# Optimization experiments

Hardware: AMD Instinct MI355X
Metric: run time of the kernel (lower is better)

The kernel has to match this reference:

```python
import jax, jax.numpy as jnp
import numpy as np

N = 4_000_000
EPS = 1e-6

# Quaternion layout: (w, x, y, z)

def _qmul(q1, q2):
    w1, v1 = q1[..., :1], q1[..., 1:]
    w2, v2 = q2[..., :1], q2[..., 1:]
    w = w1 * w2 - jnp.sum(v1 * v2, axis=-1, keepdims=True)
    v = w1 * v2 + w2 * v1 + jnp.cross(v1, v2)
    return jnp.concatenate([w, v], axis=-1)

def _qinv(q):
    # unit quaternion inverse = conjugate
    return q * jnp.array([1.0, -1.0, -1.0, -1.0], dtype=q.dtype)

def _qlog(q):
    # SO(3) log map: returns tangent vector theta * axis, shape [..., 3]
    w, v = q[..., 0], q[..., 1:]
    nv = jnp.linalg.norm(v, axis=-1)
    small = nv < EPS
    nv_safe = jnp.where(small, 1.0, nv)
    theta = 2.0 * jnp.arctan2(nv, w)
    # small-angle limit: theta/nv -> 2/w
    scale = jnp.where(small, 2.0 / w, theta / nv_safe)
    return v * scale[..., None]

def setup_inputs() -> dict:
    key = jax.random.key(0)
    k1, k2 = jax.random.split(key)
    a = jax.random.normal(k1, (N, 4), dtype=jnp.float32)
    a = a / jnp.linalg.norm(a, axis=-1, keepdims=True)
    idd = jax.random.normal(k2, (N, 4), dtype=jnp.float32)
    idd = idd / jnp.linalg.norm(idd, axis=-1, keepdims=True)
    return {"a": a, "idd": idd}

def reference(a, idd):
    # (a.Inv() @ idd).Log().norm()
    rel = _qmul(_qinv(a), idd)          # [N,4] relative rotation
    tangent = _qlog(rel)                 # [N,3] log map
    return jnp.linalg.norm(tangent)      # scalar Frobenius norm
```

## Files before the change

### kernel.cpp

```cpp
#include <hip/hip_runtime.h>
#include <math.h>

#define BLOCK 256
#define UNROLL 12
#define WTILE (64 * UNROLL)

typedef float vfloat4 __attribute__((ext_vector_type(4)));

__device__ __forceinline__ float theta_sq(vfloat4 qa, vfloat4 qb) {
    float w1 = qa.x, x1 = -qa.y, y1 = -qa.z, z1 = -qa.w;
    float w2 = qb.x, x2 = qb.y,  y2 = qb.z,  z2 = qb.w;
    float w  = w1*w2 - (x1*x2 + y1*y2 + z1*z2);
    float vx = w1*x2 + w2*x1 + (y1*z2 - z1*y2);
    float vy = w1*y2 + w2*y1 + (z1*x2 - x1*z2);
    float vz = w1*z2 + w2*z1 + (x1*y2 - y1*x2);
    float nv2 = vx*vx + vy*vy + vz*vz;
    float nv  = sqrtf(nv2);
    if (nv < 1e-6f) {
        float s = 2.0f / w;
        return nv2 * s * s;
    }
    float rn = rsqrtf(w*w + nv2);
    float c  = w * rn;
    float ac = fabsf(c);
    float p  = ((-0.0187293f*ac + 0.0742610f)*ac - 0.2121144f)*ac + 1.5707288f;
    float r  = sqrtf(fmaxf(1.0f - ac, 0.0f)) * p;
    float acosc = (c >= 0.0f) ? r : (3.14159265358979f - r);
    float theta = 2.0f * acosc;
    return theta * theta;
}

__global__ __launch_bounds__(BLOCK) void geo_loss_kernel(
        const vfloat4* __restrict__ a,
        const vfloat4* __restrict__ idd,
        float* __restrict__ ws, int n) {
    const int tid  = threadIdx.x;
    const int lane = tid & 63;
    const int gw   = (blockIdx.x * BLOCK + tid) >> 6;
    const int wbase = gw * WTILE;
    float acc = 0.0f;

    if (wbase + WTILE <= n) {
        vfloat4 qa[UNROLL], qb[UNROLL];
        #pragma unroll
        for (int k = 0; k < UNROLL; k++)
            qa[k] = __builtin_nontemporal_load(&a[wbase + k * 64 + lane]);
        #pragma unroll
        for (int k = 0; k < UNROLL; k++)
            qb[k] = __builtin_nontemporal_load(&idd[wbase + k * 64 + lane]);
        #pragma unroll
        for (int k = 0; k < UNROLL; k++)
            acc += theta_sq(qa[k], qb[k]);
    } else if (wbase < n) {
        for (int k = 0; k < UNROLL; k++) {
            int idx = wbase + k * 64 + lane;
            if (idx < n) acc += theta_sq(a[idx], idd[idx]);
        }
    }

    #pragma unroll
    for (int off = 32; off > 0; off >>= 1)
        acc += __shfl_down(acc, off, 64);
    __shared__ float smem[BLOCK / 64];
    int wid = tid >> 6;
    if (lane == 0) smem[wid] = acc;
    __syncthreads();
    if (tid == 0) {
        float s = smem[0] + smem[1] + smem[2] + smem[3];
        atomicAdd(ws, s);
    }
}

__global__ void finalize_kernel(const float* __restrict__ ws,
                                float* __restrict__ out) {
    out[0] = sqrtf(ws[0]);
}

extern "C" void kernel_launch(void* const* d_in, const int* in_sizes, int n_in,
                              void* d_out, int out_size, void* d_ws, size_t ws_size,
                              hipStream_t stream) {
    const vfloat4* a   = (const vfloat4*)d_in[0];
    const vfloat4* idd = (const vfloat4*)d_in[1];
    int n = in_sizes[0] / 4;
    float* ws = (float*)d_ws;

    (void)hipMemsetAsync(ws, 0, sizeof(float), stream);

    int nwaves = (n + WTILE - 1) / WTILE;
    int grid   = (nwaves + (BLOCK / 64) - 1) / (BLOCK / 64);
    geo_loss_kernel<<<grid, BLOCK, 0, stream>>>(a, idd, ws, n);
    finalize_kernel<<<1, 1, 0, stream>>>(ws, (float*)d_out);
}
```

Baseline: 145.5 us.

## Replace atomic accumulation with per-block partials and drop memset and nontemporal loads

Each block now writes its partial sum to its own workspace slot instead of doing an atomicAdd on a single float. A 256-thread finalize kernel then reduces all partials and takes the square root. This removes the hipMemsetAsync launch and the contention on one atomic address. Loads also switch from nontemporal vector loads to plain float4 loads, which changes the cache policy on the streamed inputs.

```diff
diff --git a/kernel.cpp b/kernel.cpp
--- a/kernel.cpp
+++ b/kernel.cpp
@@ -5,9 +5,7 @@
 #define UNROLL 12
 #define WTILE (64 * UNROLL)
 
-typedef float vfloat4 __attribute__((ext_vector_type(4)));
-
-__device__ __forceinline__ float theta_sq(vfloat4 qa, vfloat4 qb) {
+__device__ __forceinline__ float theta_sq(float4 qa, float4 qb) {
     float w1 = qa.x, x1 = -qa.y, y1 = -qa.z, z1 = -qa.w;
     float w2 = qb.x, x2 = qb.y,  y2 = qb.z,  z2 = qb.w;
     float w  = w1*w2 - (x1*x2 + y1*y2 + z1*z2);
@@ -31,9 +29,9 @@
 }
 
 __global__ __launch_bounds__(BLOCK) void geo_loss_kernel(
-        const vfloat4* __restrict__ a,
-        const vfloat4* __restrict__ idd,
-        float* __restrict__ ws, int n) {
+        const float4* __restrict__ a,
+        const float4* __restrict__ idd,
+        float* __restrict__ partials, int n) {
     const int tid  = threadIdx.x;
     const int lane = tid & 63;
     const int gw   = (blockIdx.x * BLOCK + tid) >> 6;
@@ -41,16 +39,13 @@
     float acc = 0.0f;
 
     if (wbase + WTILE <= n) {
-        vfloat4 qa[UNROLL], qb[UNROLL];
+        float4 qa[UNROLL], qb[UNROLL];
         #pragma unroll
-        for (int k = 0; k < UNROLL; k++)
-            qa[k] = __builtin_nontemporal_load(&a[wbase + k * 64 + lane]);
+        for (int k = 0; k < UNROLL; k++) qa[k] = a[wbase + k * 64 + lane];
         #pragma unroll
-        for (int k = 0; k < UNROLL; k++)
-            qb[k] = __builtin_nontemporal_load(&idd[wbase + k * 64 + lane]);
+        for (int k = 0; k < UNROLL; k++) qb[k] = idd[wbase + k * 64 + lane];
         #pragma unroll
-        for (int k = 0; k < UNROLL; k++)
-            acc += theta_sq(qa[k], qb[k]);
+        for (int k = 0; k < UNROLL; k++) acc += theta_sq(qa[k], qb[k]);
     } else if (wbase < n) {
         for (int k = 0; k < UNROLL; k++) {
             int idx = wbase + k * 64 + lane;
@@ -65,29 +60,38 @@
     int wid = tid >> 6;
     if (lane == 0) smem[wid] = acc;
     __syncthreads();
-    if (tid == 0) {
-        float s = smem[0] + smem[1] + smem[2] + smem[3];
-        atomicAdd(ws, s);
-    }
+    if (tid == 0)
+        partials[blockIdx.x] = smem[0] + smem[1] + smem[2] + smem[3];
 }
 
-__global__ void finalize_kernel(const float* __restrict__ ws,
-                                float* __restrict__ out) {
-    out[0] = sqrtf(ws[0]);
+__global__ __launch_bounds__(BLOCK) void finalize_kernel(
+        const float* __restrict__ partials,
+        float* __restrict__ out, int nparts) {
+    float acc = 0.0f;
+    for (int i = threadIdx.x; i < nparts; i += BLOCK)
+        acc += partials[i];
+    #pragma unroll
+    for (int off = 32; off > 0; off >>= 1)
+        acc += __shfl_down(acc, off, 64);
+    __shared__ float smem[BLOCK / 64];
+    int lane = threadIdx.x & 63;
+    int wid  = threadIdx.x >> 6;
+    if (lane == 0) smem[wid] = acc;
+    __syncthreads();
+    if (threadIdx.x == 0)
+        out[0] = sqrtf(smem[0] + smem[1] + smem[2] + smem[3]);
 }
 
 extern "C" void kernel_launch(void* const* d_in, const int* in_sizes, int n_in,
                               void* d_out, int out_size, void* d_ws, size_t ws_size,
                               hipStream_t stream) {
-    const vfloat4* a   = (const vfloat4*)d_in[0];
-    const vfloat4* idd = (const vfloat4*)d_in[1];
+    const float4* a   = (const float4*)d_in[0];
+    const float4* idd = (const float4*)d_in[1];
     int n = in_sizes[0] / 4;
     float* ws = (float*)d_ws;
-
-    (void)hipMemsetAsync(ws, 0, sizeof(float), stream);
 
     int nwaves = (n + WTILE - 1) / WTILE;
     int grid   = (nwaves + (BLOCK / 64) - 1) / (BLOCK / 64);
     geo_loss_kernel<<<grid, BLOCK, 0, stream>>>(a, idd, ws, n);
-    finalize_kernel<<<1, 1, 0, stream>>>(ws, (float*)d_out);
+    finalize_kernel<<<1, BLOCK, 0, stream>>>(ws, (float*)d_out, grid);
 }
```

After: 144.6 us. Within noise of the previous version (-0.6%).
